# Kernel optimization log

Measured on AMD Instinct MI355X. Metric: run time of the kernel, lower is better.

## Reference

```python
import jax, jax.numpy as jnp
import numpy as np


def _dwconv(x, w, pad):
    # depthwise conv, NCHW, weight (C,1,kh,kw), feature_group_count=C
    return jax.lax.conv_general_dilated(
        x, w, window_strides=(1, 1), padding=pad,
        feature_group_count=x.shape[1],
        dimension_numbers=('NCHW', 'OIHW', 'NCHW'))


def _max_channel_relu(x):
    # assumed MaxChannelReLU: keep only the channel-max value at each (b,h,w)
    return x * (x == jnp.max(x, axis=1, keepdims=True))


def setup_inputs() -> dict:
    key = jax.random.key(0)
    ks = jax.random.split(key, 6)
    B, C, H, W = 16, 64, 128, 128
    x = jax.random.normal(ks[0], (B, C, H, W), dtype=jnp.float32)
    w_bbx = 0.1 * jax.random.normal(ks[1], (C, 1, 1, 1), dtype=jnp.float32)
    w_width = 0.1 * jax.random.normal(ks[2], (C, 1, 1, 11), dtype=jnp.float32)
    w_width_sh = 0.1 * jax.random.normal(ks[3], (C, 1, 1, 1), dtype=jnp.float32)
    w_height = 0.1 * jax.random.normal(ks[4], (C, 1, 11, 1), dtype=jnp.float32)
    w_height_sh = 0.1 * jax.random.normal(ks[5], (C, 1, 1, 1), dtype=jnp.float32)
    return {"x": x, "w_bbx": w_bbx, "w_width": w_width,
            "w_width_sh": w_width_sh, "w_height": w_height,
            "w_height_sh": w_height_sh}


def reference(x, w_bbx, w_width, w_width_sh, w_height, w_height_sh):
    B, C, H, W = x.shape
    # self.bbx: depthwise 1x1 conv == per-channel scale
    wh = x * w_bbx.reshape(1, C, 1, 1)
    # width branch: depthwise (1,11) conv pad 5, scaled by W, then shared 1x1
    w = _dwconv(wh, w_width, [(0, 0), (5, 5)]) * W
    w = w * w_width_sh.reshape(1, C, 1, 1)
    # height branch: depthwise (11,1) conv pad 5, scaled by H, then shared 1x1
    h = _dwconv(wh, w_height, [(5, 5), (0, 0)]) * H
    h = h * w_height_sh.reshape(1, C, 1, 1)
    sx = jax.nn.sigmoid(x)
    M = jnp.max(sx, axis=(-2, -1), keepdims=True) - 0.01
    score = x * (sx > M).astype(x.dtype)
    S = jnp.sum(score, axis=(-2, -1), keepdims=True)
    sn = score / S  # normalized weights, reused by all weighted reductions
    ws = jnp.sum(w * sn, axis=(-2, -1))
    hs = jnp.sum(h * sn, axis=(-2, -1))
    ps = jnp.max(sx, axis=(-2, -1))
    col = jnp.arange(W, dtype=x.dtype).reshape(1, 1, 1, W)
    row = jnp.arange(H, dtype=x.dtype).reshape(1, 1, H, 1)
    x1 = jnp.sum(col * sn, axis=(-2, -1)) - ws / 2
    y1 = jnp.sum(row * sn, axis=(-2, -1)) - hs / 2
    x2 = x1 + ws
    y2 = y1 + hs
    score_m = _max_channel_relu(score)
    w_m = _max_channel_relu(w)
    h_m = _max_channel_relu(h)
    i = jnp.broadcast_to(jnp.arange(B, dtype=x.dtype)[:, None], (B, C))
    bbox = jnp.stack([i, x1, y1, x2, y2, ps], axis=-1).reshape(-1, 6)
    return jnp.concatenate([score_m, w_m, h_m], axis=1), bbox
```

## Files before the change

kernel.cpp:

```cpp
#include <hip/hip_runtime.h>
#include <math.h>

#define BATCH 16
#define CH    64
#define HH    128
#define WW    128
#define PLANE (HH*WW)
#define LROW  144
#define LROWS 138
#define OUT0  (BATCH*3*CH*PLANE)
#define SR4   36
#define SROWS 26
#define MBOFF 8192
#define MBN   786432


__device__ __forceinline__ unsigned enc32(float f) {
    unsigned u = __float_as_uint(f);
    return (u & 0x80000000u) ? ~u : (u | 0x80000000u);
}
__device__ __forceinline__ float dec32(unsigned k) {
    unsigned u = (k & 0x80000000u) ? (k ^ 0x80000000u) : ~k;
    return __uint_as_float(u);
}

__global__ __launch_bounds__(256) void k_stats(
    const float* __restrict__ x,
    const float* __restrict__ w_bbx, const float* __restrict__ w_width,
    const float* __restrict__ w_width_sh, const float* __restrict__ w_height,
    const float* __restrict__ w_height_sh,
    float* __restrict__ ws) {
    __shared__ float xs[LROWS * LROW];
    __shared__ float red[4 * 5];
    __shared__ float sm[5];
    int bid = blockIdx.x;
    int b = bid >> 6, c = bid & 63;
    (void)b;
    int tid = threadIdx.x;

    for (int j = tid; j < LROWS * LROW / 4; j += 256)
        ((float4*)xs)[j] = make_float4(0.f, 0.f, 0.f, 0.f);
    __syncthreads();
    const float* xp = x + (size_t)bid * PLANE;
    float m = -INFINITY;
#pragma unroll
    for (int i = 0; i < 16; i++) {
        int idx = i * 256 + tid;
        int p = idx * 4;
        int y = p >> 7, xc = p & 127;
        float4 v = ((const float4*)xp)[idx];
        m = fmaxf(m, fmaxf(fmaxf(v.x, v.y), fmaxf(v.z, v.w)));
        *(float4*)&xs[(y + 5) * LROW + xc + 8] = v;
    }
#pragma unroll
    for (int off = 32; off; off >>= 1) m = fmaxf(m, __shfl_xor(m, off, 64));
    int wid = tid >> 6, lane = tid & 63;
    if (lane == 0) sm[wid] = m;
    __syncthreads();
    if (tid == 0) {
        float mm = fmaxf(fmaxf(sm[0], sm[1]), fmaxf(sm[2], sm[3]));
        float ps = 1.0f / (1.0f + expf(-mm));
        ws[bid] = ps - 0.01f;
        ws[1024 + bid] = ps;
        sm[4] = ps - 0.01f;
    }
    float wk[11], hk[11];
#pragma unroll
    for (int k = 0; k < 11; k++) {
        wk[k] = w_width[c * 11 + k];
        hk[k] = w_height[c * 11 + k];
    }
    float cb = w_bbx[c];
    float cw = 128.0f * w_width_sh[c] * cb;
    float chs = 128.0f * w_height_sh[c] * cb;
    __syncthreads();
    float M = sm[4];

    float S = 0.f, Sw = 0.f, Sh = 0.f, Scol = 0.f, Srow = 0.f;
    for (int g = 0; g < 16; g++) {
        int idx = g * 256 + tid;
        int p = idx * 4;
        int y = p >> 7, xc = p & 127;
        float4 vx;
        float hx = 0.f, hy = 0.f, hz = 0.f, hw = 0.f;
#pragma unroll
        for (int k = 0; k < 11; k++) {
            float4 v = *(const float4*)&xs[(y + k) * LROW + xc + 8];
            if (k == 5) vx = v;
            hx += v.x * hk[k]; hy += v.y * hk[k];
            hz += v.z * hk[k]; hw += v.w * hk[k];
        }
        float wbuf[20];
        {
            float4 a0 = *(const float4*)&xs[(y + 5) * LROW + xc + 0];
            float4 a1 = *(const float4*)&xs[(y + 5) * LROW + xc + 4];
            float4 a3 = *(const float4*)&xs[(y + 5) * LROW + xc + 12];
            float4 a4 = *(const float4*)&xs[(y + 5) * LROW + xc + 16];
            wbuf[0] = a0.x;  wbuf[1] = a0.y;  wbuf[2] = a0.z;  wbuf[3] = a0.w;
            wbuf[4] = a1.x;  wbuf[5] = a1.y;  wbuf[6] = a1.z;  wbuf[7] = a1.w;
            wbuf[8] = vx.x;  wbuf[9] = vx.y;  wbuf[10] = vx.z; wbuf[11] = vx.w;
            wbuf[12] = a3.x; wbuf[13] = a3.y; wbuf[14] = a3.z; wbuf[15] = a3.w;
            wbuf[16] = a4.x; wbuf[17] = a4.y; wbuf[18] = a4.z; wbuf[19] = a4.w;
        }
        float wo[4];
#pragma unroll
        for (int j = 0; j < 4; j++) {
            float acc = 0.f;
#pragma unroll
            for (int k = 0; k < 11; k++) acc += wbuf[j + 3 + k] * wk[k];
            wo[j] = acc * cw;
        }
        float ho[4] = {hx * chs, hy * chs, hz * chs, hw * chs};
        float xv[4] = {vx.x, vx.y, vx.z, vx.w};
        float sc[4];
#pragma unroll
        for (int j = 0; j < 4; j++) {
            float sx = 1.0f / (1.0f + expf(-xv[j]));
            sc[j] = (sx > M) ? xv[j] : 0.0f;
        }
        float s4 = sc[0] + sc[1] + sc[2] + sc[3];
        S += s4;
        Srow += (float)y * s4;
#pragma unroll
        for (int j = 0; j < 4; j++) {
            Sw += wo[j] * sc[j];
            Sh += ho[j] * sc[j];
            Scol += (float)(xc + j) * sc[j];
        }
    }
#pragma unroll
    for (int off = 32; off; off >>= 1) {
        S    += __shfl_xor(S, off, 64);
        Sw   += __shfl_xor(Sw, off, 64);
        Sh   += __shfl_xor(Sh, off, 64);
        Scol += __shfl_xor(Scol, off, 64);
        Srow += __shfl_xor(Srow, off, 64);
    }
    if (lane == 0) {
        red[wid * 5 + 0] = S;   red[wid * 5 + 1] = Sw;
        red[wid * 5 + 2] = Sh;  red[wid * 5 + 3] = Scol;
        red[wid * 5 + 4] = Srow;
    }
    __syncthreads();
    if (tid == 0) {
        float a0 = 0, a1 = 0, a2 = 0, a3 = 0, a4 = 0;
#pragma unroll
        for (int w2 = 0; w2 < 4; w2++) {
            a0 += red[w2 * 5 + 0]; a1 += red[w2 * 5 + 1];
            a2 += red[w2 * 5 + 2]; a3 += red[w2 * 5 + 3];
            a4 += red[w2 * 5 + 4];
        }
        ws[2048 + bid] = a0;
        ws[3072 + bid] = a1;
        ws[4096 + bid] = a2;
        ws[5120 + bid] = a3;
        ws[6144 + bid] = a4;
    }
}

__global__ __launch_bounds__(512) void k_maxch(
    const float* __restrict__ x,
    const float* __restrict__ w_bbx, const float* __restrict__ w_width,
    const float* __restrict__ w_width_sh, const float* __restrict__ w_height,
    const float* __restrict__ w_height_sh,
    const float* __restrict__ ws, unsigned long long* __restrict__ mb) {
    __shared__ float4 xs4[2][SROWS * SR4];
    int t = blockIdx.x;
    int half = blockIdx.y;
    int b = blockIdx.z;
    int tid = threadIdx.x;
    int r = tid >> 5, q = tid & 31;

    for (int j = tid; j < 2 * SROWS * SR4; j += 512)
        ((float4*)xs4)[j] = make_float4(0.f, 0.f, 0.f, 0.f);

    int cbase = half * 32;
    {
        const float* xp = x + (size_t)(b * 64 + cbase) * PLANE;
        for (int j = tid; j < SROWS * 32; j += 512) {
            int i = j >> 5, c4 = j & 31;
            int gr = t * 16 - 5 + i;
            float4 v = make_float4(0.f, 0.f, 0.f, 0.f);
            if ((unsigned)gr < 128u) v = ((const float4*)xp)[gr * 32 + c4];
            xs4[0][i * SR4 + 2 + c4] = v;
        }
    }
    unsigned long long kW[4], kH[4], kS[4];
#pragma unroll
    for (int j = 0; j < 4; j++) { kW[j] = 0ull; kH[j] = 0ull; kS[j] = 0ull; }

    int cur = 0;
    for (int cc = 0; cc < 32; cc++) {
        __syncthreads();
        int c = cbase + cc;
        float4 p0 = make_float4(0.f, 0.f, 0.f, 0.f);
        float4 p1 = make_float4(0.f, 0.f, 0.f, 0.f);
        bool have = (cc + 1 < 32);
        if (have) {
            const float* xp = x + (size_t)(b * 64 + c + 1) * PLANE;
            int i0 = tid >> 5, c40 = tid & 31;
            int gr0 = t * 16 - 5 + i0;
            if ((unsigned)gr0 < 128u) p0 = ((const float4*)xp)[gr0 * 32 + c40];
            if (tid < 320) {
                int gr1 = gr0 + 16;
                if ((unsigned)gr1 < 128u) p1 = ((const float4*)xp)[gr1 * 32 + c40];
            }
        }
        float wkc[11], hkc[11];
#pragma unroll
        for (int k = 0; k < 11; k++) {
            wkc[k] = w_width[c * 11 + k];
            hkc[k] = w_height[c * 11 + k];
        }
        float cb = w_bbx[c];
        float cw = 128.0f * w_width_sh[c] * cb;
        float chs = 128.0f * w_height_sh[c] * cb;
        float M = ws[b * 64 + c];

        float4 vx;
        float hx = 0.f, hy = 0.f, hz = 0.f, hw = 0.f;
#pragma unroll
        for (int k = 0; k < 11; k++) {
            float4 v = xs4[cur][(r + k) * SR4 + 2 + q];
            if (k == 5) vx = v;
            hx += v.x * hkc[k]; hy += v.y * hkc[k];
            hz += v.z * hkc[k]; hw += v.w * hkc[k];
        }
        float wbuf[20];
        {
            float4 a0 = xs4[cur][(r + 5) * SR4 + q + 0];
            float4 a1 = xs4[cur][(r + 5) * SR4 + q + 1];
            float4 a3 = xs4[cur][(r + 5) * SR4 + q + 3];
            float4 a4 = xs4[cur][(r + 5) * SR4 + q + 4];
            wbuf[0] = a0.x;  wbuf[1] = a0.y;  wbuf[2] = a0.z;  wbuf[3] = a0.w;
            wbuf[4] = a1.x;  wbuf[5] = a1.y;  wbuf[6] = a1.z;  wbuf[7] = a1.w;
            wbuf[8] = vx.x;  wbuf[9] = vx.y;  wbuf[10] = vx.z; wbuf[11] = vx.w;
            wbuf[12] = a3.x; wbuf[13] = a3.y; wbuf[14] = a3.z; wbuf[15] = a3.w;
            wbuf[16] = a4.x; wbuf[17] = a4.y; wbuf[18] = a4.z; wbuf[19] = a4.w;
        }
        float wo[4];
#pragma unroll
        for (int j = 0; j < 4; j++) {
            float acc = 0.f;
#pragma unroll
            for (int k = 0; k < 11; k++) acc += wbuf[j + 3 + k] * wkc[k];
            wo[j] = acc * cw;
        }
        float ho[4] = {hx * chs, hy * chs, hz * chs, hw * chs};
        float xv[4] = {vx.x, vx.y, vx.z, vx.w};
#pragma unroll
        for (int j = 0; j < 4; j++) {
            float sx = 1.0f / (1.0f + expf(-xv[j]));
            float sc = (sx > M) ? xv[j] : 0.0f;
            unsigned long long cand;
            cand = ((unsigned long long)enc32(sc) << 32) | (unsigned)c;
            if (cand > kS[j]) kS[j] = cand;
            cand = ((unsigned long long)enc32(wo[j]) << 32) | (unsigned)c;
            if (cand > kW[j]) kW[j] = cand;
            cand = ((unsigned long long)enc32(ho[j]) << 32) | (unsigned)c;
            if (cand > kH[j]) kH[j] = cand;
        }
        if (have) {
            xs4[cur ^ 1][(tid >> 5) * SR4 + 2 + (tid & 31)] = p0;
            if (tid < 320)
                xs4[cur ^ 1][((tid >> 5) + 16) * SR4 + 2 + (tid & 31)] = p1;
        }
        cur ^= 1;
    }
    int gr = t * 16 + r;
    size_t pix = (size_t)gr * 128 + 4 * q;
    unsigned long long* o = mb + (size_t)half * MBN;
    size_t i0 = (size_t)(b * 3 + 0) * 16384 + pix;
    size_t i1 = (size_t)(b * 3 + 1) * 16384 + pix;
    size_t i2 = (size_t)(b * 3 + 2) * 16384 + pix;
#pragma unroll
    for (int j = 0; j < 4; j++) {
        o[i0 + j] = kS[j];
        o[i1 + j] = kW[j];
        o[i2 + j] = kH[j];
    }
}

__global__ __launch_bounds__(256) void k_scatter(
    const unsigned long long* __restrict__ mb, float* __restrict__ out) {
    int chunk = blockIdx.x;
    int f = blockIdx.y;
    int b = blockIdx.z;
    int tid = threadIdx.x;
    size_t pix = (size_t)chunk * 1024 + tid * 4;
    size_t ki = (size_t)(b * 3 + f) * 16384 + pix;
    const unsigned long long* m0 = mb;
    const unsigned long long* m1 = mb + MBN;
    float val[4];
    int win[4];
#pragma unroll
    for (int j = 0; j < 4; j++) {
        unsigned long long k0 = m0[ki + j], k1 = m1[ki + j];
        unsigned long long k = (k0 > k1) ? k0 : k1;
        val[j] = dec32((unsigned)(k >> 32));
        win[j] = (int)(k & 63u);
    }
    float* ob = out + (size_t)(b * 192 + f * 64) * PLANE + pix;
#pragma unroll
    for (int c = 0; c < 64; c++) {
        float4 o;
        o.x = (win[0] == c) ? val[0] : 0.f;
        o.y = (win[1] == c) ? val[1] : 0.f;
        o.z = (win[2] == c) ? val[2] : 0.f;
        o.w = (win[3] == c) ? val[3] : 0.f;
        *(float4*)&ob[(size_t)c * PLANE] = o;
    }
}

__global__ __launch_bounds__(256) void k_bbox(const float* __restrict__ ws,
                                              float* __restrict__ out) {
    int idx = blockIdx.x * 256 + threadIdx.x;
    if (idx >= 1024) return;
    int b = idx >> 6;
    float S    = ws[2048 + idx];
    float Sw   = ws[3072 + idx];
    float Sh   = ws[4096 + idx];
    float Scol = ws[5120 + idx];
    float Srow = ws[6144 + idx];
    float ps   = ws[1024 + idx];
    float inv = 1.0f / S;
    float wsv = Sw * inv, hsv = Sh * inv;
    float x1 = Scol * inv - 0.5f * wsv;
    float y1 = Srow * inv - 0.5f * hsv;
    float* o = out + OUT0 + (size_t)idx * 6;
    o[0] = (float)b;
    o[1] = x1;
    o[2] = y1;
    o[3] = x1 + wsv;
    o[4] = y1 + hsv;
    o[5] = ps;
}

extern "C" void kernel_launch(void* const* d_in, const int* in_sizes, int n_in,
                              void* d_out, int out_size, void* d_ws, size_t ws_size,
                              hipStream_t stream) {
    const float* x          = (const float*)d_in[0];
    const float* w_bbx      = (const float*)d_in[1];
    const float* w_width    = (const float*)d_in[2];
    const float* w_width_sh = (const float*)d_in[3];
    const float* w_height   = (const float*)d_in[4];
    const float* w_height_sh= (const float*)d_in[5];
    float* out = (float*)d_out;
    float* ws  = (float*)d_ws;
    unsigned long long* mb = (unsigned long long*)(ws + MBOFF);

    k_stats<<<dim3(1024), dim3(256), 0, stream>>>(
        x, w_bbx, w_width, w_width_sh, w_height, w_height_sh, ws);
    k_maxch<<<dim3(8, 2, 16), dim3(512), 0, stream>>>(
        x, w_bbx, w_width, w_width_sh, w_height, w_height_sh, ws, mb);
    k_scatter<<<dim3(16, 3, 16), dim3(256), 0, stream>>>(mb, out);
    k_bbox<<<dim3(4), dim3(256), 0, stream>>>(ws, out);
}
```

Measured before the change: 362.0 us.

## Fold weighted sums into channel-max conv kernel and merge partials via atomicMax

The stats kernel no longer recomputes both convolutions per plane. It now only computes the per-plane max and zeroes the argmax buffer. The weighted sums (S, Sw, Sh, Scol, Srow) are accumulated inside the channel-max conv kernel as per-tile partials, and the bbox kernel reduces those partials. The conv grid is retiled to 8-row tiles and 16-channel groups (more blocks, 256 threads), and the packed value/channel keys are combined with 64-bit atomicMax instead of two half buffers. This removes a second full read and conv pass over x, at the cost of extra halo rows, per-channel wave reductions, atomics and a mid-kernel reduction buffer.

```diff
diff --git a/kernel.cpp b/kernel.cpp
--- a/kernel.cpp
+++ b/kernel.cpp
@@ -6,13 +6,12 @@
 #define HH    128
 #define WW    128
 #define PLANE (HH*WW)
-#define LROW  144
-#define LROWS 138
 #define OUT0  (BATCH*3*CH*PLANE)
-#define SR4   36
-#define SROWS 26
-#define MBOFF 8192
-#define MBN   786432
+#define SR4    36
+#define TSROWS 18
+#define PART_OFF 2048
+#define MB_OFF   90112
+#define MB_N     786432
 
 
 __device__ __forceinline__ unsigned enc32(float f) {
@@ -24,36 +23,25 @@
     return __uint_as_float(u);
 }
 
-__global__ __launch_bounds__(256) void k_stats(
-    const float* __restrict__ x,
-    const float* __restrict__ w_bbx, const float* __restrict__ w_width,
-    const float* __restrict__ w_width_sh, const float* __restrict__ w_height,
-    const float* __restrict__ w_height_sh,
-    float* __restrict__ ws) {
-    __shared__ float xs[LROWS * LROW];
-    __shared__ float red[4 * 5];
-    __shared__ float sm[5];
+__global__ __launch_bounds__(256) void k_max(const float* __restrict__ x,
+                                             float* __restrict__ ws,
+                                             unsigned long long* __restrict__ mb) {
     int bid = blockIdx.x;
-    int b = bid >> 6, c = bid & 63;
-    (void)b;
     int tid = threadIdx.x;
-
-    for (int j = tid; j < LROWS * LROW / 4; j += 256)
-        ((float4*)xs)[j] = make_float4(0.f, 0.f, 0.f, 0.f);
-    __syncthreads();
-    const float* xp = x + (size_t)bid * PLANE;
+    {
+        size_t base = (size_t)bid * 768 + tid;
+        mb[base] = 0ull; mb[base + 256] = 0ull; mb[base + 512] = 0ull;
+    }
+    const float4* xp = (const float4*)(x + (size_t)bid * PLANE);
     float m = -INFINITY;
 #pragma unroll
     for (int i = 0; i < 16; i++) {
-        int idx = i * 256 + tid;
-        int p = idx * 4;
-        int y = p >> 7, xc = p & 127;
-        float4 v = ((const float4*)xp)[idx];
+        float4 v = xp[i * 256 + tid];
         m = fmaxf(m, fmaxf(fmaxf(v.x, v.y), fmaxf(v.z, v.w)));
-        *(float4*)&xs[(y + 5) * LROW + xc + 8] = v;
     }
 #pragma unroll
     for (int off = 32; off; off >>= 1) m = fmaxf(m, __shfl_xor(m, off, 64));
+    __shared__ float sm[4];
     int wid = tid >> 6, lane = tid & 63;
     if (lane == 0) sm[wid] = m;
     __syncthreads();
@@ -62,124 +50,34 @@
         float ps = 1.0f / (1.0f + expf(-mm));
         ws[bid] = ps - 0.01f;
         ws[1024 + bid] = ps;
-        sm[4] = ps - 0.01f;
-    }
-    float wk[11], hk[11];
-#pragma unroll
-    for (int k = 0; k < 11; k++) {
-        wk[k] = w_width[c * 11 + k];
-        hk[k] = w_height[c * 11 + k];
-    }
-    float cb = w_bbx[c];
-    float cw = 128.0f * w_width_sh[c] * cb;
-    float chs = 128.0f * w_height_sh[c] * cb;
-    __syncthreads();
-    float M = sm[4];
-
-    float S = 0.f, Sw = 0.f, Sh = 0.f, Scol = 0.f, Srow = 0.f;
-    for (int g = 0; g < 16; g++) {
-        int idx = g * 256 + tid;
-        int p = idx * 4;
-        int y = p >> 7, xc = p & 127;
-        float4 vx;
-        float hx = 0.f, hy = 0.f, hz = 0.f, hw = 0.f;
-#pragma unroll
-        for (int k = 0; k < 11; k++) {
-            float4 v = *(const float4*)&xs[(y + k) * LROW + xc + 8];
-            if (k == 5) vx = v;
-            hx += v.x * hk[k]; hy += v.y * hk[k];
-            hz += v.z * hk[k]; hw += v.w * hk[k];
-        }
-        float wbuf[20];
-        {
-            float4 a0 = *(const float4*)&xs[(y + 5) * LROW + xc + 0];
-            float4 a1 = *(const float4*)&xs[(y + 5) * LROW + xc + 4];
-            float4 a3 = *(const float4*)&xs[(y + 5) * LROW + xc + 12];
-            float4 a4 = *(const float4*)&xs[(y + 5) * LROW + xc + 16];
-            wbuf[0] = a0.x;  wbuf[1] = a0.y;  wbuf[2] = a0.z;  wbuf[3] = a0.w;
-            wbuf[4] = a1.x;  wbuf[5] = a1.y;  wbuf[6] = a1.z;  wbuf[7] = a1.w;
-            wbuf[8] = vx.x;  wbuf[9] = vx.y;  wbuf[10] = vx.z; wbuf[11] = vx.w;
-            wbuf[12] = a3.x; wbuf[13] = a3.y; wbuf[14] = a3.z; wbuf[15] = a3.w;
-            wbuf[16] = a4.x; wbuf[17] = a4.y; wbuf[18] = a4.z; wbuf[19] = a4.w;
-        }
-        float wo[4];
-#pragma unroll
-        for (int j = 0; j < 4; j++) {
-            float acc = 0.f;
-#pragma unroll
-            for (int k = 0; k < 11; k++) acc += wbuf[j + 3 + k] * wk[k];
-            wo[j] = acc * cw;
-        }
-        float ho[4] = {hx * chs, hy * chs, hz * chs, hw * chs};
-        float xv[4] = {vx.x, vx.y, vx.z, vx.w};
-        float sc[4];
-#pragma unroll
-        for (int j = 0; j < 4; j++) {
-            float sx = 1.0f / (1.0f + expf(-xv[j]));
-            sc[j] = (sx > M) ? xv[j] : 0.0f;
-        }
-        float s4 = sc[0] + sc[1] + sc[2] + sc[3];
-        S += s4;
-        Srow += (float)y * s4;
-#pragma unroll
-        for (int j = 0; j < 4; j++) {
-            Sw += wo[j] * sc[j];
-            Sh += ho[j] * sc[j];
-            Scol += (float)(xc + j) * sc[j];
-        }
-    }
-#pragma unroll
-    for (int off = 32; off; off >>= 1) {
-        S    += __shfl_xor(S, off, 64);
-        Sw   += __shfl_xor(Sw, off, 64);
-        Sh   += __shfl_xor(Sh, off, 64);
-        Scol += __shfl_xor(Scol, off, 64);
-        Srow += __shfl_xor(Srow, off, 64);
-    }
-    if (lane == 0) {
-        red[wid * 5 + 0] = S;   red[wid * 5 + 1] = Sw;
-        red[wid * 5 + 2] = Sh;  red[wid * 5 + 3] = Scol;
-        red[wid * 5 + 4] = Srow;
-    }
-    __syncthreads();
-    if (tid == 0) {
-        float a0 = 0, a1 = 0, a2 = 0, a3 = 0, a4 = 0;
-#pragma unroll
-        for (int w2 = 0; w2 < 4; w2++) {
-            a0 += red[w2 * 5 + 0]; a1 += red[w2 * 5 + 1];
-            a2 += red[w2 * 5 + 2]; a3 += red[w2 * 5 + 3];
-            a4 += red[w2 * 5 + 4];
-        }
-        ws[2048 + bid] = a0;
-        ws[3072 + bid] = a1;
-        ws[4096 + bid] = a2;
-        ws[5120 + bid] = a3;
-        ws[6144 + bid] = a4;
-    }
-}
-
-__global__ __launch_bounds__(512) void k_maxch(
+    }
+}
+
+__global__ __launch_bounds__(256, 4) void k_conv(
     const float* __restrict__ x,
     const float* __restrict__ w_bbx, const float* __restrict__ w_width,
     const float* __restrict__ w_width_sh, const float* __restrict__ w_height,
     const float* __restrict__ w_height_sh,
-    const float* __restrict__ ws, unsigned long long* __restrict__ mb) {
-    __shared__ float4 xs4[2][SROWS * SR4];
+    const float* __restrict__ ws, float* __restrict__ wsums,
+    unsigned long long* __restrict__ mb) {
+    __shared__ float4 xs4[2][TSROWS * SR4];
+    __shared__ float red[16 * 4 * 5];
     int t = blockIdx.x;
-    int half = blockIdx.y;
+    int g = blockIdx.y;
     int b = blockIdx.z;
     int tid = threadIdx.x;
     int r = tid >> 5, q = tid & 31;
-
-    for (int j = tid; j < 2 * SROWS * SR4; j += 512)
+    int wid = tid >> 6, lane = tid & 63;
+
+    for (int j = tid; j < 2 * TSROWS * SR4; j += 256)
         ((float4*)xs4)[j] = make_float4(0.f, 0.f, 0.f, 0.f);
-
-    int cbase = half * 32;
+    __syncthreads();
+    int cbase = g * 16;
     {
         const float* xp = x + (size_t)(b * 64 + cbase) * PLANE;
-        for (int j = tid; j < SROWS * 32; j += 512) {
+        for (int j = tid; j < TSROWS * 32; j += 256) {
             int i = j >> 5, c4 = j & 31;
-            int gr = t * 16 - 5 + i;
+            int gr = t * 8 - 5 + i;
             float4 v = make_float4(0.f, 0.f, 0.f, 0.f);
             if ((unsigned)gr < 128u) v = ((const float4*)xp)[gr * 32 + c4];
             xs4[0][i * SR4 + 2 + c4] = v;
@@ -190,20 +88,23 @@
     for (int j = 0; j < 4; j++) { kW[j] = 0ull; kH[j] = 0ull; kS[j] = 0ull; }
 
     int cur = 0;
-    for (int cc = 0; cc < 32; cc++) {
+    for (int cc = 0; cc < 16; cc++) {
         __syncthreads();
         int c = cbase + cc;
         float4 p0 = make_float4(0.f, 0.f, 0.f, 0.f);
         float4 p1 = make_float4(0.f, 0.f, 0.f, 0.f);
-        bool have = (cc + 1 < 32);
+        float4 p2 = make_float4(0.f, 0.f, 0.f, 0.f);
+        bool have = (cc + 1 < 16);
         if (have) {
             const float* xp = x + (size_t)(b * 64 + c + 1) * PLANE;
-            int i0 = tid >> 5, c40 = tid & 31;
-            int gr0 = t * 16 - 5 + i0;
-            if ((unsigned)gr0 < 128u) p0 = ((const float4*)xp)[gr0 * 32 + c40];
-            if (tid < 320) {
-                int gr1 = gr0 + 16;
-                if ((unsigned)gr1 < 128u) p1 = ((const float4*)xp)[gr1 * 32 + c40];
+            int i0 = tid >> 5, c4 = tid & 31;
+            int g0 = t * 8 - 5 + i0;
+            if ((unsigned)g0 < 128u) p0 = ((const float4*)xp)[g0 * 32 + c4];
+            int g1 = g0 + 8;
+            if ((unsigned)g1 < 128u) p1 = ((const float4*)xp)[g1 * 32 + c4];
+            if (tid < 64) {
+                int g2 = g0 + 16;
+                if ((unsigned)g2 < 128u) p2 = ((const float4*)xp)[g2 * 32 + c4];
             }
         }
         float wkc[11], hkc[11];
@@ -248,10 +149,15 @@
         }
         float ho[4] = {hx * chs, hy * chs, hz * chs, hw * chs};
         float xv[4] = {vx.x, vx.y, vx.z, vx.w};
+        float S = 0.f, Sw = 0.f, Sh = 0.f, Scol = 0.f, Srow = 0.f;
 #pragma unroll
         for (int j = 0; j < 4; j++) {
             float sx = 1.0f / (1.0f + expf(-xv[j]));
             float sc = (sx > M) ? xv[j] : 0.0f;
+            S += sc;
+            Sw += wo[j] * sc;
+            Sh += ho[j] * sc;
+            Scol += (float)(4 * q + j) * sc;
             unsigned long long cand;
             cand = ((unsigned long long)enc32(sc) << 32) | (unsigned)c;
             if (cand > kS[j]) kS[j] = cand;
@@ -260,24 +166,45 @@
             cand = ((unsigned long long)enc32(ho[j]) << 32) | (unsigned)c;
             if (cand > kH[j]) kH[j] = cand;
         }
+        Srow = (float)(t * 8 + r) * S;
+#pragma unroll
+        for (int off = 32; off; off >>= 1) {
+            S    += __shfl_xor(S, off, 64);
+            Sw   += __shfl_xor(Sw, off, 64);
+            Sh   += __shfl_xor(Sh, off, 64);
+            Scol += __shfl_xor(Scol, off, 64);
+            Srow += __shfl_xor(Srow, off, 64);
+        }
+        if (lane == 0) {
+            float* rr = &red[(cc * 4 + wid) * 5];
+            rr[0] = S; rr[1] = Sw; rr[2] = Sh; rr[3] = Scol; rr[4] = Srow;
+        }
         if (have) {
-            xs4[cur ^ 1][(tid >> 5) * SR4 + 2 + (tid & 31)] = p0;
-            if (tid < 320)
-                xs4[cur ^ 1][((tid >> 5) + 16) * SR4 + 2 + (tid & 31)] = p1;
+            int i0 = tid >> 5, c4 = tid & 31;
+            xs4[cur ^ 1][i0 * SR4 + 2 + c4] = p0;
+            xs4[cur ^ 1][(i0 + 8) * SR4 + 2 + c4] = p1;
+            if (tid < 64) xs4[cur ^ 1][(i0 + 16) * SR4 + 2 + c4] = p2;
         }
         cur ^= 1;
     }
-    int gr = t * 16 + r;
+    __syncthreads();
+    if (tid < 80) {
+        int cc = tid / 5, j = tid % 5;
+        float s = red[(cc * 4 + 0) * 5 + j] + red[(cc * 4 + 1) * 5 + j]
+                + red[(cc * 4 + 2) * 5 + j] + red[(cc * 4 + 3) * 5 + j];
+        int c = cbase + cc;
+        wsums[(((size_t)(b * 64 + c)) * 16 + t) * 5 + j] = s;
+    }
+    int gr = t * 8 + r;
     size_t pix = (size_t)gr * 128 + 4 * q;
-    unsigned long long* o = mb + (size_t)half * MBN;
     size_t i0 = (size_t)(b * 3 + 0) * 16384 + pix;
     size_t i1 = (size_t)(b * 3 + 1) * 16384 + pix;
     size_t i2 = (size_t)(b * 3 + 2) * 16384 + pix;
 #pragma unroll
     for (int j = 0; j < 4; j++) {
-        o[i0 + j] = kS[j];
-        o[i1 + j] = kW[j];
-        o[i2 + j] = kH[j];
+        atomicMax(&mb[i0 + j], kS[j]);
+        atomicMax(&mb[i1 + j], kW[j]);
+        atomicMax(&mb[i2 + j], kH[j]);
     }
 }
 
@@ -289,14 +216,11 @@
     int tid = threadIdx.x;
     size_t pix = (size_t)chunk * 1024 + tid * 4;
     size_t ki = (size_t)(b * 3 + f) * 16384 + pix;
-    const unsigned long long* m0 = mb;
-    const unsigned long long* m1 = mb + MBN;
     float val[4];
     int win[4];
 #pragma unroll
     for (int j = 0; j < 4; j++) {
-        unsigned long long k0 = m0[ki + j], k1 = m1[ki + j];
-        unsigned long long k = (k0 > k1) ? k0 : k1;
+        unsigned long long k = mb[ki + j];
         val[j] = dec32((unsigned)(k >> 32));
         win[j] = (int)(k & 63u);
     }
@@ -317,12 +241,17 @@
     int idx = blockIdx.x * 256 + threadIdx.x;
     if (idx >= 1024) return;
     int b = idx >> 6;
-    float S    = ws[2048 + idx];
-    float Sw   = ws[3072 + idx];
-    float Sh   = ws[4096 + idx];
-    float Scol = ws[5120 + idx];
-    float Srow = ws[6144 + idx];
-    float ps   = ws[1024 + idx];
+    const float* p = ws + PART_OFF + (size_t)idx * 80;
+    float S = 0.f, Sw = 0.f, Sh = 0.f, Scol = 0.f, Srow = 0.f;
+#pragma unroll
+    for (int t = 0; t < 16; t++) {
+        S    += p[t * 5 + 0];
+        Sw   += p[t * 5 + 1];
+        Sh   += p[t * 5 + 2];
+        Scol += p[t * 5 + 3];
+        Srow += p[t * 5 + 4];
+    }
+    float ps = ws[1024 + idx];
     float inv = 1.0f / S;
     float wsv = Sw * inv, hsv = Sh * inv;
     float x1 = Scol * inv - 0.5f * wsv;
@@ -347,12 +276,12 @@
     const float* w_height_sh= (const float*)d_in[5];
     float* out = (float*)d_out;
     float* ws  = (float*)d_ws;
-    unsigned long long* mb = (unsigned long long*)(ws + MBOFF);
-
-    k_stats<<<dim3(1024), dim3(256), 0, stream>>>(
-        x, w_bbx, w_width, w_width_sh, w_height, w_height_sh, ws);
-    k_maxch<<<dim3(8, 2, 16), dim3(512), 0, stream>>>(
-        x, w_bbx, w_width, w_width_sh, w_height, w_height_sh, ws, mb);
+    unsigned long long* mb = (unsigned long long*)(ws + MB_OFF);
+
+    k_max<<<dim3(1024), dim3(256), 0, stream>>>(x, ws, mb);
+    k_conv<<<dim3(16, 4, 16), dim3(256), 0, stream>>>(
+        x, w_bbx, w_width, w_width_sh, w_height, w_height_sh,
+        ws, ws + PART_OFF, mb);
     k_scatter<<<dim3(16, 3, 16), dim3(256), 0, stream>>>(mb, out);
     k_bbox<<<dim3(4), dim3(256), 0, stream>>>(ws, out);
 }
```

After: 453.2 us. 1.25x slower.
